# Kernel optimization log

Hardware: AMD Instinct MI355X
Metric: run time of the kernel (lower is better)

The kernel has to match this reference:

```python
import jax, jax.numpy as jnp
import numpy as np

N = 1_000_000   # total points
C = 20          # semantic classes
B = 4           # scenes in batch
L = 200         # instance label vocabulary
INST = 64       # number of proposals/instances
M = 300_000     # masked points (len(object_idxs))
T = 320_000     # total proposal rows
IGNORE = -100
PREPARE_EPOCHS = 128


def setup_inputs() -> dict:
    key = jax.random.key(0)
    ks = jax.random.split(key, 12)
    semantic_scores = jax.random.normal(ks[0], (N, C), jnp.float32)
    semantic_labels = jax.random.randint(ks[1], (N,), 0, C)
    lab = jax.random.randint(ks[2], (N,), 0, L)
    ign = jax.random.uniform(ks[3], (N,)) < 0.05
    instance_labels = jnp.where(ign, IGNORE, lab)
    pt_offsets = jax.random.normal(ks[4], (N, 3), jnp.float32)
    instance_info = jax.random.normal(ks[5], (N, 9), jnp.float32)
    coords = jax.random.normal(ks[6], (N, 3), jnp.float32)
    mask_logits = jax.random.normal(ks[7], (INST, M), jnp.float32)
    object_idxs = jax.random.randint(ks[8], (M,), 0, N)
    col1 = jax.random.randint(ks[9], (T,), 0, N)
    proposals_idx_shift = jnp.stack([jnp.zeros_like(col1), col1], axis=1)
    mids = jnp.sort(jax.random.randint(ks[10], (INST - 1,), 0, T))
    proposals_offset_shift = jnp.concatenate(
        [jnp.zeros((1,), jnp.int32), mids.astype(jnp.int32), jnp.full((1,), T, jnp.int32)])
    inst_batch_ids = jax.random.randint(ks[11], (INST,), 0, B)
    batch_offsets = jnp.array([0, N // 4, N // 2, 3 * N // 4, N], dtype=jnp.int32)
    batch_ids = jnp.clip(jnp.searchsorted(batch_offsets, object_idxs, side='right') - 1, 0, B - 1)
    inst_pred_seg_label = jax.random.randint(jax.random.fold_in(key, 99), (INST,), 0, C)
    return dict(semantic_scores=semantic_scores, pt_offsets=pt_offsets,
                instance_info=instance_info, coords=coords, mask_logits=mask_logits,
                semantic_labels=semantic_labels, instance_labels=instance_labels,
                object_idxs=object_idxs, proposals_idx_shift=proposals_idx_shift,
                proposals_offset_shift=proposals_offset_shift, inst_batch_ids=inst_batch_ids,
                batch_ids=batch_ids, batch_offsets=batch_offsets,
                inst_pred_seg_label=inst_pred_seg_label, epoch=200)


def reference(semantic_scores, pt_offsets, instance_info, coords, mask_logits,
              semantic_labels, instance_labels, object_idxs, proposals_idx_shift,
              proposals_offset_shift, inst_batch_ids, batch_ids, batch_offsets,
              inst_pred_seg_label, epoch):
    f32 = jnp.float32
    n_pts = semantic_scores.shape[0]
    n_inst, m_pts = mask_logits.shape
    n_batch = batch_offsets.shape[0] - 1
    LW = L + 1  # label buckets, bucket 0 == ignore(-100)

    # --- semantic cross entropy (ignore_index) ---
    logp = jax.nn.log_softmax(semantic_scores, axis=-1)
    sem_valid = semantic_labels != IGNORE
    safe_lab = jnp.where(sem_valid, semantic_labels, 0)
    nll = -jnp.take_along_axis(logp, safe_lab[:, None], axis=1)[:, 0]
    semantic_loss = jnp.sum(nll * sem_valid) / jnp.maximum(jnp.sum(sem_valid), 1)

    # --- offset losses ---
    gt_offsets = instance_info[:, 0:3] - coords
    pt_dist = jnp.sum(jnp.abs(pt_offsets - gt_offsets), axis=-1)
    valid = (instance_labels != IGNORE).astype(f32)
    vsum = jnp.sum(valid) + 1e-6
    offset_norm_loss = jnp.sum(pt_dist * valid) / vsum
    gt_u = gt_offsets / (jnp.linalg.norm(gt_offsets, axis=1, keepdims=True) + 1e-8)
    pt_u = pt_offsets / (jnp.linalg.norm(pt_offsets, axis=1, keepdims=True) + 1e-8)
    offset_dir_loss = jnp.sum(-jnp.sum(gt_u * pt_u, axis=-1) * valid) / vsum

    loss = semantic_loss + offset_norm_loss + offset_dir_loss

    if epoch > PREPARE_EPOCHS:
        # map instance labels to ids: ignore -> 0, label l -> l+1 (order-preserving, so
        # argmax-first tie-break == torch.mode smallest-value tie-break)
        labels_id = jnp.where(instance_labels == IGNORE, 0, instance_labels + 1)
        # segment id per proposal row from CSR offsets
        seg = jnp.clip(jnp.searchsorted(proposals_offset_shift, jnp.arange(T), side='right') - 1,
                       0, n_inst - 1)
        prop_lab = labels_id[proposals_idx_shift[:, 1]]
        hist = jax.ops.segment_sum(jnp.ones((T,), f32), seg * LW + prop_lab,
                                   num_segments=n_inst * LW).reshape(n_inst, LW)
        mode_id = jnp.argmax(hist, axis=1)                       # [INST] per-instance mode vote

        masked_lab = labels_id[object_idxs]                      # [M]
        sem_masked = semantic_labels[object_idxs]                # [M]
        skip = (mode_id == 0) | (inst_pred_seg_label <= 3)       # [INST]

        batch_match = inst_batch_ids[:, None] == batch_ids[None, :]           # [INST,M]
        sem_match = inst_pred_seg_label[:, None] == sem_masked[None, :]       # [INST,M]
        weights = batch_match.astype(f32) * jnp.where(skip[:, None], 1.0,
                                                      sem_match.astype(f32))  # [INST,M]

        # per-batch label histograms (full points and masked points)
        point_batch = jnp.clip(jnp.searchsorted(batch_offsets, jnp.arange(n_pts),
                                                side='right') - 1, 0, n_batch - 1)
        hist_full = jax.ops.segment_sum(jnp.ones((n_pts,), f32), point_batch * LW + labels_id,
                                        num_segments=n_batch * LW).reshape(n_batch, LW)
        hist_mask = jax.ops.segment_sum(jnp.ones((m_pts,), f32), batch_ids * LW + masked_lab,
                                        num_segments=n_batch * LW).reshape(n_batch, LW)
        num = hist_mask[inst_batch_ids, mode_id]
        den = hist_full[inst_batch_ids, mode_id]
        cover = jnp.where(den > 0, num / den, 0.0)
        pos = (~skip) & (cover > 0.3)
        inst_gt_mask = (pos[:, None] & (masked_lab[None, :] == mode_id[:, None])).astype(f32)

        pred = jax.nn.sigmoid(mask_logits)
        wb = (weights > 0).astype(f32)
        inter = jnp.sum(wb * pred * inst_gt_mask, axis=1)
        union = jnp.sum(wb * pred * pred, axis=1) + jnp.sum(wb * inst_gt_mask * inst_gt_mask, axis=1) + 1e-5
        dice_n = 1.0 - 2.0 * inter / union
        dice_valid = (~skip) & (jnp.sum(wb, axis=1) > 0)
        dice_loss = jnp.sum(jnp.where(dice_valid, dice_n, 0.0)) / (jnp.sum(dice_valid.astype(f32)) + 1e-6)

        # BCE(sigmoid(x), t) in stable form: softplus(x) - t*x
        bce = jax.nn.softplus(mask_logits) - inst_gt_mask * mask_logits
        score_loss = jnp.sum(bce * weights) / (jnp.sum(weights) + 1e-6)

        loss = loss + score_loss + dice_loss
    return loss
```

## Files before the change

### kernel.cpp

```cpp
#include <hip/hip_runtime.h>
#include <math.h>

namespace {

constexpr int N_PTS  = 1000000;
constexpr int C_CLS  = 20;
constexpr int N_B    = 4;
constexpr int L_LAB  = 200;
constexpr int LW     = L_LAB + 1;
constexpr int N_INST = 64;
constexpr int M_PTS  = 300000;
constexpr int T_PROP = 320000;
constexpr int IGN    = -100;
constexpr int PREP   = 128;

constexpr size_t OFF_G      = 0;
constexpr size_t OFF_INTER  = 64;
constexpr size_t OFF_UP     = 576;
constexpr size_t OFF_UG     = 1088;
constexpr size_t OFF_WBS    = 1600;
constexpr size_t OFF_SN     = 2112;
constexpr size_t OFF_HFULL  = 2624;
constexpr size_t OFF_HMASK  = 5840;
constexpr size_t OFF_IHIST  = 9056;
constexpr size_t OFF_FLAGS  = 60512;
constexpr size_t ZERO_BYTES = 60768;
constexpr size_t OFF_META   = 60800;
constexpr size_t WS_REQUIRED = OFF_META + (size_t)M_PTS * 2;

__device__ __forceinline__ float waveSumF(float v) {
  #pragma unroll
  for (int off = 32; off > 0; off >>= 1) v += __shfl_down(v, off, 64);
  return v;
}
__device__ __forceinline__ int waveMaxI(int v) {
  #pragma unroll
  for (int off = 32; off > 0; off >>= 1) v = max(v, __shfl_down(v, off, 64));
  return v;
}

constexpr int PB_PT   = 1024;
constexpr int PB_HF   = 256;
constexpr int PB_PROP = 256;
constexpr int PB_HM   = 256;
constexpr int A_BLOCKS = PB_PT + PB_HF + PB_PROP + PB_HM;

__global__ __launch_bounds__(256) void k_A(const float* __restrict__ scores,
                                           const float* __restrict__ pt_off,
                                           const float* __restrict__ info,
                                           const float* __restrict__ coords,
                                           const int* __restrict__ sem_lab,
                                           const int* __restrict__ inst_lab,
                                           const int* __restrict__ obj_idx,
                                           const int* __restrict__ batch_ids,
                                           const int* __restrict__ prop_idx,
                                           const int* __restrict__ prop_off,
                                           const int* __restrict__ batch_off,
                                           double* __restrict__ g,
                                           int* __restrict__ hist_full,
                                           int* __restrict__ hist_mask,
                                           int* __restrict__ inst_hist,
                                           unsigned short* __restrict__ meta,
                                           int write_meta) {
  __shared__ float4 shbuf4[4 * 320];
  int*   sh  = reinterpret_cast<int*>(shbuf4);
  float* shf = reinterpret_cast<float*>(shbuf4);
  const int bx = blockIdx.x;

  if (bx < PB_PT) {
    const int lane = threadIdx.x & 63, wv = threadIdx.x >> 6;
    float4* shw4 = shbuf4 + wv * 320;
    float*  shwf = reinterpret_cast<float*>(shw4);
    float s_nll = 0.f, s_cnt = 0.f, s_dist = 0.f, s_dir = 0.f, s_val = 0.f;

    constexpr int NT      = N_PTS / 64;
    constexpr int TSTRIDE = PB_PT * 4;
    const int base = bx * 4 + wv;
    const int nit = (NT - bx * 4 + TSTRIDE - 1) / TSTRIDE;

    for (int it = 0; it < nit; ++it) {
      const int tile = base + it * TSTRIDE;
      const bool act = tile < NT;
      int sl = 0, il = IGN;

      if (act) {
        const int p = tile * 64 + lane;
        sl = sem_lab[p];
        il = inst_lab[p];
        const float4* s4 = reinterpret_cast<const float4*>(scores) + (size_t)tile * 320;
        #pragma unroll
        for (int r = 0; r < 5; ++r) shw4[r * 64 + lane] = s4[r * 64 + lane];
      }
      __syncthreads();

      if (act) {
        float mx = -3.4e38f;
        #pragma unroll
        for (int r = 0; r < 5; ++r) {
          const float4 a = shw4[lane * 5 + r];
          mx = fmaxf(mx, fmaxf(fmaxf(a.x, a.y), fmaxf(a.z, a.w)));
        }
        float se = 0.f;
        #pragma unroll
        for (int r = 0; r < 5; ++r) {
          const float4 a = shw4[lane * 5 + r];
          se += __expf(a.x - mx) + __expf(a.y - mx) + __expf(a.z - mx) + __expf(a.w - mx);
        }
        const float xs = shwf[lane * 20 + ((sl == IGN) ? 0 : sl)];
        if (sl != IGN) { s_nll += (mx + __logf(se)) - xs; s_cnt += 1.f; }
      }
      __syncthreads();

      if (act) {
        const float4* c4 = reinterpret_cast<const float4*>(coords) + (size_t)tile * 48;
        const float4* o4 = reinterpret_cast<const float4*>(pt_off) + (size_t)tile * 48;
        const float4* i4 = reinterpret_cast<const float4*>(info)   + (size_t)tile * 144;
        if (lane < 48) { shw4[lane] = c4[lane]; shw4[48 + lane] = o4[lane]; }
        shw4[96 + lane]  = i4[lane];
        shw4[160 + lane] = i4[64 + lane];
        if (lane < 16) shw4[224 + lane] = i4[128 + lane];
      }
      __syncthreads();

      if (act && il != IGN) {
        const float cx = shwf[3 * lane + 0], cy = shwf[3 * lane + 1], cz = shwf[3 * lane + 2];
        const float ox = shwf[192 + 3 * lane + 0], oy = shwf[192 + 3 * lane + 1], oz = shwf[192 + 3 * lane + 2];
        const float gx = shwf[384 + 9 * lane + 0] - cx;
        const float gy = shwf[384 + 9 * lane + 1] - cy;
        const float gz = shwf[384 + 9 * lane + 2] - cz;
        s_val  += 1.f;
        s_dist += fabsf(ox - gx) + fabsf(oy - gy) + fabsf(oz - gz);
        const float gn = sqrtf(gx * gx + gy * gy + gz * gz) + 1e-8f;
        const float pn = sqrtf(ox * ox + oy * oy + oz * oz) + 1e-8f;
        s_dir += -((gx * ox + gy * oy + gz * oz) / (gn * pn));
      }
      __syncthreads();
    }

    float vals[5] = { s_nll, s_cnt, s_dist, s_dir, s_val };
    #pragma unroll
    for (int k = 0; k < 5; ++k) {
      const float t = waveSumF(vals[k]);
      if (lane == 0) shf[k * 4 + wv] = t;
    }
    __syncthreads();
    if (threadIdx.x < 5) {
      const float s = shf[threadIdx.x * 4 + 0] + shf[threadIdx.x * 4 + 1] +
                      shf[threadIdx.x * 4 + 2] + shf[threadIdx.x * 4 + 3];
      atomicAdd(&g[threadIdx.x], (double)s);
    }
  } else if (bx < PB_PT + PB_HF) {
    for (int t = threadIdx.x; t < N_B * LW; t += blockDim.x) sh[t] = 0;
    __syncthreads();
    const int b1 = batch_off[1], b2 = batch_off[2], b3 = batch_off[3];
    const int blk = bx - PB_PT;
    const int4* il4p = reinterpret_cast<const int4*>(inst_lab);
    const int nq = N_PTS / 4;
    for (int q = blk * blockDim.x + threadIdx.x; q < nq; q += PB_HF * blockDim.x) {
      const int4 v = il4p[q];
      const int p = q * 4;
      const int ils[4] = { v.x, v.y, v.z, v.w };
      #pragma unroll
      for (int k = 0; k < 4; ++k) {
        const int lab = (ils[k] == IGN) ? 0 : (ils[k] + 1);
        const int pp = p + k;
        int pb = 0;
        if (pp >= b1) pb = 1;
        if (pp >= b2) pb = 2;
        if (pp >= b3) pb = 3;
        atomicAdd(&sh[pb * LW + lab], 1);
      }
    }
    __syncthreads();
    for (int t = threadIdx.x; t < N_B * LW; t += blockDim.x)
      if (sh[t]) atomicAdd(&hist_full[t], sh[t]);
  } else if (bx < PB_PT + PB_HF + PB_PROP) {
    if (threadIdx.x <= N_INST) sh[threadIdx.x] = prop_off[threadIdx.x];
    __syncthreads();
    const int blk = bx - PB_PT - PB_HF;
    const int4* pi4 = reinterpret_cast<const int4*>(prop_idx);
    const int nq = T_PROP / 2;
    for (int q = blk * blockDim.x + threadIdx.x; q < nq; q += PB_PROP * blockDim.x) {
      const int4 v = pi4[q];
      const int t0 = 2 * q, t1 = 2 * q + 1;
      const int il0 = inst_lab[v.y];
      const int il1 = inst_lab[v.w];
      int lo0 = 0, hi0 = N_INST + 1, lo1 = 0, hi1 = N_INST + 1;
      #pragma unroll
      for (int s = 0; s < 7; ++s) {
        const int m0 = (lo0 + hi0) >> 1;
        if (m0 <= N_INST && sh[m0] <= t0) lo0 = m0 + 1; else hi0 = m0;
        const int m1 = (lo1 + hi1) >> 1;
        if (m1 <= N_INST && sh[m1] <= t1) lo1 = m1 + 1; else hi1 = m1;
      }
      const int seg0 = min(lo0 - 1, N_INST - 1);
      const int seg1 = min(lo1 - 1, N_INST - 1);
      const int lab0 = (il0 == IGN) ? 0 : (il0 + 1);
      const int lab1 = (il1 == IGN) ? 0 : (il1 + 1);
      atomicAdd(&inst_hist[seg0 * LW + lab0], 1);
      atomicAdd(&inst_hist[seg1 * LW + lab1], 1);
    }
  } else {
    for (int t = threadIdx.x; t < N_B * LW; t += blockDim.x) sh[t] = 0;
    __syncthreads();
    const int blk = bx - PB_PT - PB_HF - PB_PROP;
    const int4* oi4 = reinterpret_cast<const int4*>(obj_idx);
    const int4* bi4 = reinterpret_cast<const int4*>(batch_ids);
    ushort4* m4 = reinterpret_cast<ushort4*>(meta);
    const int nq = M_PTS / 4;
    for (int q = blk * blockDim.x + threadIdx.x; q < nq; q += PB_HM * blockDim.x) {
      const int4 o = oi4[q];
      const int4 b = bi4[q];
      const int il0 = inst_lab[o.x], il1 = inst_lab[o.y],
                il2 = inst_lab[o.z], il3 = inst_lab[o.w];
      const int sm0 = sem_lab[o.x], sm1 = sem_lab[o.y],
                sm2 = sem_lab[o.z], sm3 = sem_lab[o.w];
      const int ml0 = (il0 == IGN) ? 0 : (il0 + 1);
      const int ml1 = (il1 == IGN) ? 0 : (il1 + 1);
      const int ml2 = (il2 == IGN) ? 0 : (il2 + 1);
      const int ml3 = (il3 == IGN) ? 0 : (il3 + 1);
      atomicAdd(&sh[b.x * LW + ml0], 1);
      atomicAdd(&sh[b.y * LW + ml1], 1);
      atomicAdd(&sh[b.z * LW + ml2], 1);
      atomicAdd(&sh[b.w * LW + ml3], 1);
      if (write_meta) {
        ushort4 mm;
        mm.x = (unsigned short)(ml0 | (sm0 << 8) | (b.x << 13));
        mm.y = (unsigned short)(ml1 | (sm1 << 8) | (b.y << 13));
        mm.z = (unsigned short)(ml2 | (sm2 << 8) | (b.z << 13));
        mm.w = (unsigned short)(ml3 | (sm3 << 8) | (b.w << 13));
        m4[q] = mm;
      }
    }
    __syncthreads();
    for (int t = threadIdx.x; t < N_B * LW; t += blockDim.x)
      if (sh[t]) atomicAdd(&hist_mask[t], sh[t]);
  }
}

__global__ __launch_bounds__(256) void k_argmax(const int* __restrict__ inst_hist,
                                                const int* __restrict__ hist_full,
                                                const int* __restrict__ hist_mask,
                                                const int* __restrict__ inst_batch_ids,
                                                const int* __restrict__ inst_seg,
                                                int* __restrict__ flags) {
  __shared__ int red[4];
  const int i = blockIdx.x;
  const int t = threadIdx.x;
  int key = 0;
  if (t < LW) {
    const int cnt = inst_hist[i * LW + t];
    key = (cnt << 8) | (255 - t);
  }
  key = waveMaxI(key);
  const int lane = t & 63, wv = t >> 6;
  if (lane == 0) red[wv] = key;
  __syncthreads();
  if (t == 0) {
    int k = max(max(red[0], red[1]), max(red[2], red[3]));
    const int m = 255 - (k & 0xFF);
    const int b = inst_batch_ids[i];
    const int seg = inst_seg[i];
    const bool skip = (m == 0) || (seg <= 3);
    const float num = (float)hist_mask[b * LW + m];
    const float den = (float)hist_full[b * LW + m];
    const float cover = (den > 0.f) ? (num / den) : 0.f;
    const bool pos = (!skip) && (cover > 0.3f);
    flags[i] = m | (skip ? 0x100 : 0) | (pos ? 0x200 : 0) | (b << 10) | (seg << 12);
  }
}

template <bool USE_META>
__global__ __launch_bounds__(256) void k_mask(const float* __restrict__ logits,
                                              const unsigned short* __restrict__ meta,
                                              const int* __restrict__ obj_idx,
                                              const int* __restrict__ inst_lab,
                                              const int* __restrict__ sem_lab,
                                              const int* __restrict__ batch_ids,
                                              const int* __restrict__ flags,
                                              double* __restrict__ i_inter,
                                              double* __restrict__ i_up,
                                              double* __restrict__ i_ug,
                                              double* __restrict__ i_wbs,
                                              double* __restrict__ i_sn) {
  const int i  = blockIdx.y;
  const int fl = flags[i];
  const int  mode_i = fl & 0xFF;
  const bool skip   = (fl >> 8) & 1;
  const bool pos    = (fl >> 9) & 1;
  const int  bi     = (fl >> 10) & 3;
  const int  seg    = (fl >> 12) & 31;

  float inter = 0.f, up = 0.f, ug = 0.f, wbs = 0.f, sn = 0.f;

  if (USE_META) {
    const float4* row4 = reinterpret_cast<const float4*>(logits + (size_t)i * M_PTS);
    const ushort4* m4  = reinterpret_cast<const ushort4*>(meta);
    const int nq = M_PTS / 4;
    for (int q = blockIdx.x * blockDim.x + threadIdx.x; q < nq; q += gridDim.x * blockDim.x) {
      const float4  x4 = row4[q];
      const ushort4 d4 = m4[q];
      const float xs[4] = { x4.x, x4.y, x4.z, x4.w };
      const int   ds[4] = { d4.x, d4.y, d4.z, d4.w };
      #pragma unroll
      for (int k = 0; k < 4; ++k) {
        const int md = ds[k];
        const int ml = md & 0xFF;
        const int sm = (md >> 8) & 31;
        const int b  = (md >> 13) & 3;
        const bool w  = (b == bi) && (skip || (sm == seg));
        const bool gt = pos && (ml == mode_i);
        const float x  = xs[k];
        const float e  = __expf(-fabsf(x));
        const float r  = __builtin_amdgcn_rcpf(1.f + e);
        const float pr = (x >= 0.f) ? r : e * r;
        const float sp = fmaxf(x, 0.f) + __logf(1.f + e);
        const float wf = w ? 1.f : 0.f;
        const float gf = gt ? 1.f : 0.f;
        up    += wf * pr * pr;
        wbs   += wf;
        sn    += wf * (sp - gf * x);
        inter += wf * gf * pr;
        ug    += wf * gf;
      }
    }
  } else {
    const float* row = logits + (size_t)i * M_PTS;
    for (int j = blockIdx.x * blockDim.x + threadIdx.x; j < M_PTS; j += gridDim.x * blockDim.x) {
      const int o  = obj_idx[j];
      const int il = inst_lab[o];
      const int ml = (il == IGN) ? 0 : (il + 1);
      const int sm = sem_lab[o];
      const int b  = batch_ids[j];
      const bool w  = (b == bi) && (skip || (sm == seg));
      const bool gt = pos && (ml == mode_i);
      const float x  = row[j];
      const float e  = __expf(-fabsf(x));
      const float r  = __builtin_amdgcn_rcpf(1.f + e);
      const float pr = (x >= 0.f) ? r : e * r;
      const float sp = fmaxf(x, 0.f) + __logf(1.f + e);
      const float wf = w ? 1.f : 0.f;
      const float gf = gt ? 1.f : 0.f;
      up    += wf * pr * pr;
      wbs   += wf;
      sn    += wf * (sp - gf * x);
      inter += wf * gf * pr;
      ug    += wf * gf;
    }
  }

  __shared__ float red[5][4];
  float vals[5] = { inter, up, ug, wbs, sn };
  const int lane = threadIdx.x & 63, wv = threadIdx.x >> 6;
  #pragma unroll
  for (int k = 0; k < 5; ++k) {
    const float t = waveSumF(vals[k]);
    if (lane == 0) red[k][wv] = t;
  }
  __syncthreads();
  if (threadIdx.x < 5) {
    const float s = red[threadIdx.x][0] + red[threadIdx.x][1] + red[threadIdx.x][2] + red[threadIdx.x][3];
    double* dst = (threadIdx.x == 0) ? (i_inter + i)
                : (threadIdx.x == 1) ? (i_up + i)
                : (threadIdx.x == 2) ? (i_ug + i)
                : (threadIdx.x == 3) ? (i_wbs + i)
                                     : (i_sn + i);
    atomicAdd(dst, (double)s);
  }
}

__global__ __launch_bounds__(64) void k_final(const double* __restrict__ g,
                                              const double* __restrict__ i_inter,
                                              const double* __restrict__ i_up,
                                              const double* __restrict__ i_ug,
                                              const double* __restrict__ i_wbs,
                                              const double* __restrict__ i_sn,
                                              const int* __restrict__ flags,
                                              const int* __restrict__ epoch,
                                              float* __restrict__ out) {
  const int i = threadIdx.x;
  const bool act = epoch[0] > PREP;
  double sn = 0.0, wsum = 0.0, dice = 0.0, dcnt = 0.0;
  if (act) {
    wsum = i_wbs[i];
    sn   = i_sn[i];
    const bool skip = (flags[i] >> 8) & 1;
    if (!skip && wsum > 0.0) {
      const double un = i_up[i] + i_ug[i] + 1e-5;
      dice = 1.0 - 2.0 * i_inter[i] / un;
      dcnt = 1.0;
    }
    #pragma unroll
    for (int off = 32; off > 0; off >>= 1) {
      wsum += __shfl_down(wsum, off, 64);
      sn   += __shfl_down(sn,   off, 64);
      dice += __shfl_down(dice, off, 64);
      dcnt += __shfl_down(dcnt, off, 64);
    }
  }
  if (i == 0) {
    double loss = g[0] / fmax(g[1], 1.0);
    const double vsum = g[4] + 1e-6;
    loss += g[2] / vsum + g[3] / vsum;
    if (act) loss += sn / (wsum + 1e-6) + dice / (dcnt + 1e-6);
    out[0] = (float)loss;
  }
}

}

extern "C" void kernel_launch(void* const* d_in, const int* in_sizes, int n_in,
                              void* d_out, int out_size, void* d_ws, size_t ws_size,
                              hipStream_t stream) {
  const float* semantic_scores  = (const float*)d_in[0];
  const float* pt_offsets       = (const float*)d_in[1];
  const float* instance_info    = (const float*)d_in[2];
  const float* coords           = (const float*)d_in[3];
  const float* mask_logits      = (const float*)d_in[4];
  const int*   semantic_labels  = (const int*)d_in[5];
  const int*   instance_labels  = (const int*)d_in[6];
  const int*   object_idxs      = (const int*)d_in[7];
  const int*   proposals_idx    = (const int*)d_in[8];
  const int*   proposals_off    = (const int*)d_in[9];
  const int*   inst_batch_ids   = (const int*)d_in[10];
  const int*   batch_ids        = (const int*)d_in[11];
  const int*   batch_offsets    = (const int*)d_in[12];
  const int*   inst_seg         = (const int*)d_in[13];
  const int*   epoch            = (const int*)d_in[14];
  float* out = (float*)d_out;

  char* w = (char*)d_ws;
  double* g        = (double*)(w + OFF_G);
  double* i_inter  = (double*)(w + OFF_INTER);
  double* i_up     = (double*)(w + OFF_UP);
  double* i_ug     = (double*)(w + OFF_UG);
  double* i_wbs    = (double*)(w + OFF_WBS);
  double* i_sn     = (double*)(w + OFF_SN);
  int* hist_full   = (int*)(w + OFF_HFULL);
  int* hist_mask   = (int*)(w + OFF_HMASK);
  int* inst_hist   = (int*)(w + OFF_IHIST);
  int* flags       = (int*)(w + OFF_FLAGS);
  unsigned short* meta = (unsigned short*)(w + OFF_META);

  const bool use_meta = (ws_size >= WS_REQUIRED);

  (void)hipMemsetAsync(d_ws, 0, ZERO_BYTES, stream);

  k_A<<<A_BLOCKS, 256, 0, stream>>>(semantic_scores, pt_offsets, instance_info, coords,
                                    semantic_labels, instance_labels, object_idxs,
                                    batch_ids, proposals_idx, proposals_off, batch_offsets,
                                    g, hist_full, hist_mask, inst_hist, meta,
                                    use_meta ? 1 : 0);

  k_argmax<<<N_INST, 256, 0, stream>>>(inst_hist, hist_full, hist_mask,
                                       inst_batch_ids, inst_seg, flags);

  dim3 mgrid(40, N_INST);
  if (use_meta) {
    k_mask<true><<<mgrid, 256, 0, stream>>>(mask_logits, meta, object_idxs, instance_labels,
                                            semantic_labels, batch_ids, flags,
                                            i_inter, i_up, i_ug, i_wbs, i_sn);
  } else {
    k_mask<false><<<mgrid, 256, 0, stream>>>(mask_logits, meta, object_idxs, instance_labels,
                                             semantic_labels, batch_ids, flags,
                                             i_inter, i_up, i_ug, i_wbs, i_sn);
  }
  k_final<<<1, 64, 0, stream>>>(g, i_inter, i_up, i_ug, i_wbs, i_sn, flags, epoch, out);
}
```

Measured before the change: 273.7 us.

## Drop per-tile block barriers in point loop and replace double atomics with partials

The point-loss blocks now give each wave its own shared-memory region holding scores, coords, offsets and info together. This removes the four block-wide __syncthreads per tile, since each wave reads only its own data. Each point block writes its five partial sums to a workspace array instead of doing double-precision atomicAdds, and the final kernel grows to 256 threads to reduce those partials. Shared memory per block rises, which may lower occupancy. Correctness relies on wave-level execution ordering for the intra-wave shared-memory handoff.

```diff
diff --git a/kernel.cpp b/kernel.cpp
--- a/kernel.cpp
+++ b/kernel.cpp
@@ -25,7 +25,10 @@
 constexpr size_t OFF_IHIST  = 9056;
 constexpr size_t OFF_FLAGS  = 60512;
 constexpr size_t ZERO_BYTES = 60768;
-constexpr size_t OFF_META   = 60800;
+constexpr size_t OFF_PART   = 60800;
+constexpr size_t PART_BYTES = 5 * 1024 * 4;
+constexpr size_t WS_PART_REQ = OFF_PART + PART_BYTES;
+constexpr size_t OFF_META   = WS_PART_REQ;
 constexpr size_t WS_REQUIRED = OFF_META + (size_t)M_PTS * 2;
 
 __device__ __forceinline__ float waveSumF(float v) {
@@ -44,6 +47,8 @@
 constexpr int PB_PROP = 256;
 constexpr int PB_HM   = 256;
 constexpr int A_BLOCKS = PB_PT + PB_HF + PB_PROP + PB_HM;
+
+constexpr int WREG = 560;
 
 __global__ __launch_bounds__(256) void k_A(const float* __restrict__ scores,
                                            const float* __restrict__ pt_off,
@@ -57,19 +62,21 @@
                                            const int* __restrict__ prop_off,
                                            const int* __restrict__ batch_off,
                                            double* __restrict__ g,
+                                           float* __restrict__ part,
+                                           int use_part,
                                            int* __restrict__ hist_full,
                                            int* __restrict__ hist_mask,
                                            int* __restrict__ inst_hist,
                                            unsigned short* __restrict__ meta,
                                            int write_meta) {
-  __shared__ float4 shbuf4[4 * 320];
+  __shared__ float4 shbuf4[4 * WREG];
   int*   sh  = reinterpret_cast<int*>(shbuf4);
   float* shf = reinterpret_cast<float*>(shbuf4);
   const int bx = blockIdx.x;
 
   if (bx < PB_PT) {
     const int lane = threadIdx.x & 63, wv = threadIdx.x >> 6;
-    float4* shw4 = shbuf4 + wv * 320;
+    float4* shw4 = shbuf4 + wv * WREG;
     float*  shwf = reinterpret_cast<float*>(shw4);
     float s_nll = 0.f, s_cnt = 0.f, s_dist = 0.f, s_dir = 0.f, s_val = 0.f;
 
@@ -80,20 +87,22 @@
 
     for (int it = 0; it < nit; ++it) {
       const int tile = base + it * TSTRIDE;
-      const bool act = tile < NT;
-      int sl = 0, il = IGN;
-
-      if (act) {
+      if (tile < NT) {
         const int p = tile * 64 + lane;
-        sl = sem_lab[p];
-        il = inst_lab[p];
+        const int sl = sem_lab[p];
+        const int il = inst_lab[p];
+
         const float4* s4 = reinterpret_cast<const float4*>(scores) + (size_t)tile * 320;
         #pragma unroll
         for (int r = 0; r < 5; ++r) shw4[r * 64 + lane] = s4[r * 64 + lane];
-      }
-      __syncthreads();
-
-      if (act) {
+        const float4* c4 = reinterpret_cast<const float4*>(coords) + (size_t)tile * 48;
+        const float4* o4 = reinterpret_cast<const float4*>(pt_off) + (size_t)tile * 48;
+        const float4* i4 = reinterpret_cast<const float4*>(info)   + (size_t)tile * 144;
+        if (lane < 48) { shw4[320 + lane] = c4[lane]; shw4[368 + lane] = o4[lane]; }
+        shw4[416 + lane] = i4[lane];
+        shw4[480 + lane] = i4[64 + lane];
+        if (lane < 16) shw4[544 + lane] = i4[128 + lane];
+
         float mx = -3.4e38f;
         #pragma unroll
         for (int r = 0; r < 5; ++r) {
@@ -108,35 +117,27 @@
         }
         const float xs = shwf[lane * 20 + ((sl == IGN) ? 0 : sl)];
         if (sl != IGN) { s_nll += (mx + __logf(se)) - xs; s_cnt += 1.f; }
-      }
-      __syncthreads();
-
-      if (act) {
-        const float4* c4 = reinterpret_cast<const float4*>(coords) + (size_t)tile * 48;
-        const float4* o4 = reinterpret_cast<const float4*>(pt_off) + (size_t)tile * 48;
-        const float4* i4 = reinterpret_cast<const float4*>(info)   + (size_t)tile * 144;
-        if (lane < 48) { shw4[lane] = c4[lane]; shw4[48 + lane] = o4[lane]; }
-        shw4[96 + lane]  = i4[lane];
-        shw4[160 + lane] = i4[64 + lane];
-        if (lane < 16) shw4[224 + lane] = i4[128 + lane];
-      }
-      __syncthreads();
-
-      if (act && il != IGN) {
-        const float cx = shwf[3 * lane + 0], cy = shwf[3 * lane + 1], cz = shwf[3 * lane + 2];
-        const float ox = shwf[192 + 3 * lane + 0], oy = shwf[192 + 3 * lane + 1], oz = shwf[192 + 3 * lane + 2];
-        const float gx = shwf[384 + 9 * lane + 0] - cx;
-        const float gy = shwf[384 + 9 * lane + 1] - cy;
-        const float gz = shwf[384 + 9 * lane + 2] - cz;
-        s_val  += 1.f;
-        s_dist += fabsf(ox - gx) + fabsf(oy - gy) + fabsf(oz - gz);
-        const float gn = sqrtf(gx * gx + gy * gy + gz * gz) + 1e-8f;
-        const float pn = sqrtf(ox * ox + oy * oy + oz * oz) + 1e-8f;
-        s_dir += -((gx * ox + gy * oy + gz * oz) / (gn * pn));
-      }
-      __syncthreads();
-    }
-
+
+        if (il != IGN) {
+          const float cx = shwf[1280 + 3 * lane + 0];
+          const float cy = shwf[1280 + 3 * lane + 1];
+          const float cz = shwf[1280 + 3 * lane + 2];
+          const float ox = shwf[1472 + 3 * lane + 0];
+          const float oy = shwf[1472 + 3 * lane + 1];
+          const float oz = shwf[1472 + 3 * lane + 2];
+          const float gx = shwf[1664 + 9 * lane + 0] - cx;
+          const float gy = shwf[1664 + 9 * lane + 1] - cy;
+          const float gz = shwf[1664 + 9 * lane + 2] - cz;
+          s_val  += 1.f;
+          s_dist += fabsf(ox - gx) + fabsf(oy - gy) + fabsf(oz - gz);
+          const float gn = sqrtf(gx * gx + gy * gy + gz * gz) + 1e-8f;
+          const float pn = sqrtf(ox * ox + oy * oy + oz * oz) + 1e-8f;
+          s_dir += -((gx * ox + gy * oy + gz * oz) / (gn * pn));
+        }
+      }
+    }
+
+    __syncthreads();
     float vals[5] = { s_nll, s_cnt, s_dist, s_dir, s_val };
     #pragma unroll
     for (int k = 0; k < 5; ++k) {
@@ -147,7 +148,8 @@
     if (threadIdx.x < 5) {
       const float s = shf[threadIdx.x * 4 + 0] + shf[threadIdx.x * 4 + 1] +
                       shf[threadIdx.x * 4 + 2] + shf[threadIdx.x * 4 + 3];
-      atomicAdd(&g[threadIdx.x], (double)s);
+      if (use_part) part[threadIdx.x * PB_PT + bx] = s;
+      else          atomicAdd(&g[threadIdx.x], (double)s);
     }
   } else if (bx < PB_PT + PB_HF) {
     for (int t = threadIdx.x; t < N_B * LW; t += blockDim.x) sh[t] = 0;
@@ -369,40 +371,66 @@
   }
 }
 
-__global__ __launch_bounds__(64) void k_final(const double* __restrict__ g,
-                                              const double* __restrict__ i_inter,
-                                              const double* __restrict__ i_up,
-                                              const double* __restrict__ i_ug,
-                                              const double* __restrict__ i_wbs,
-                                              const double* __restrict__ i_sn,
-                                              const int* __restrict__ flags,
-                                              const int* __restrict__ epoch,
-                                              float* __restrict__ out) {
-  const int i = threadIdx.x;
+__global__ __launch_bounds__(256) void k_final(const double* __restrict__ g,
+                                               const float* __restrict__ part,
+                                               int use_part,
+                                               const double* __restrict__ i_inter,
+                                               const double* __restrict__ i_up,
+                                               const double* __restrict__ i_ug,
+                                               const double* __restrict__ i_wbs,
+                                               const double* __restrict__ i_sn,
+                                               const int* __restrict__ flags,
+                                               const int* __restrict__ epoch,
+                                               float* __restrict__ out) {
+  __shared__ double sred[5][4];
+  __shared__ double sG[5];
+  __shared__ double sI[4];
+  const int t = threadIdx.x, lane = t & 63, wv = t >> 6;
+
+  if (use_part) {
+    #pragma unroll
+    for (int c = 0; c < 5; ++c) {
+      double v = 0.0;
+      #pragma unroll
+      for (int j = 0; j < 4; ++j) v += (double)part[c * 1024 + t + j * 256];
+      #pragma unroll
+      for (int off = 32; off > 0; off >>= 1) v += __shfl_down(v, off, 64);
+      if (lane == 0) sred[c][wv] = v;
+    }
+    __syncthreads();
+    if (t < 5) sG[t] = sred[t][0] + sred[t][1] + sred[t][2] + sred[t][3];
+  } else {
+    if (t < 5) sG[t] = g[t];
+  }
+
   const bool act = epoch[0] > PREP;
-  double sn = 0.0, wsum = 0.0, dice = 0.0, dcnt = 0.0;
-  if (act) {
-    wsum = i_wbs[i];
-    sn   = i_sn[i];
-    const bool skip = (flags[i] >> 8) & 1;
-    if (!skip && wsum > 0.0) {
-      const double un = i_up[i] + i_ug[i] + 1e-5;
-      dice = 1.0 - 2.0 * i_inter[i] / un;
-      dcnt = 1.0;
-    }
-    #pragma unroll
-    for (int off = 32; off > 0; off >>= 1) {
-      wsum += __shfl_down(wsum, off, 64);
-      sn   += __shfl_down(sn,   off, 64);
-      dice += __shfl_down(dice, off, 64);
-      dcnt += __shfl_down(dcnt, off, 64);
-    }
-  }
-  if (i == 0) {
-    double loss = g[0] / fmax(g[1], 1.0);
-    const double vsum = g[4] + 1e-6;
-    loss += g[2] / vsum + g[3] / vsum;
-    if (act) loss += sn / (wsum + 1e-6) + dice / (dcnt + 1e-6);
+  if (t < 64) {
+    double sn = 0.0, wsum = 0.0, dice = 0.0, dcnt = 0.0;
+    if (act) {
+      wsum = i_wbs[t];
+      sn   = i_sn[t];
+      const bool skip = (flags[t] >> 8) & 1;
+      if (!skip && wsum > 0.0) {
+        const double un = i_up[t] + i_ug[t] + 1e-5;
+        dice = 1.0 - 2.0 * i_inter[t] / un;
+        dcnt = 1.0;
+      }
+      #pragma unroll
+      for (int off = 32; off > 0; off >>= 1) {
+        wsum += __shfl_down(wsum, off, 64);
+        sn   += __shfl_down(sn,   off, 64);
+        dice += __shfl_down(dice, off, 64);
+        dcnt += __shfl_down(dcnt, off, 64);
+      }
+    }
+    if (t == 0) { sI[0] = sn; sI[1] = wsum; sI[2] = dice; sI[3] = dcnt; }
+  }
+  __syncthreads();
+  if (t == 0) {
+    double loss = sG[0] / fmax(sG[1], 1.0);
+    const double vsum = sG[4] + 1e-6;
+    loss += sG[2] / vsum + sG[3] / vsum;
+    if (act) loss += sI[0] / (sI[1] + 1e-6) + sI[2] / (sI[3] + 1e-6);
     out[0] = (float)loss;
   }
 }
@@ -440,8 +468,10 @@
   int* hist_mask   = (int*)(w + OFF_HMASK);
   int* inst_hist   = (int*)(w + OFF_IHIST);
   int* flags       = (int*)(w + OFF_FLAGS);
+  float* part      = (float*)(w + OFF_PART);
   unsigned short* meta = (unsigned short*)(w + OFF_META);
 
+  const bool use_part = (ws_size >= WS_PART_REQ);
   const bool use_meta = (ws_size >= WS_REQUIRED);
 
   (void)hipMemsetAsync(d_ws, 0, ZERO_BYTES, stream);
@@ -449,7 +479,8 @@
   k_A<<<A_BLOCKS, 256, 0, stream>>>(semantic_scores, pt_offsets, instance_info, coords,
                                     semantic_labels, instance_labels, object_idxs,
                                     batch_ids, proposals_idx, proposals_off, batch_offsets,
-                                    g, hist_full, hist_mask, inst_hist, meta,
+                                    g, part, use_part ? 1 : 0,
+                                    hist_full, hist_mask, inst_hist, meta,
                                     use_meta ? 1 : 0);
 
   k_argmax<<<N_INST, 256, 0, stream>>>(inst_hist, hist_full, hist_mask,
@@ -465,5 +496,6 @@
                                              semantic_labels, batch_ids, flags,
                                              i_inter, i_up, i_ug, i_wbs, i_sn);
   }
-  k_final<<<1, 64, 0, stream>>>(g, i_inter, i_up, i_ug, i_wbs, i_sn, flags, epoch, out);
-}
+  k_final<<<1, 256, 0, stream>>>(g, part, use_part ? 1 : 0,
+                                 i_inter, i_up, i_ug, i_wbs, i_sn, flags, epoch, out);
+}
```

Result: slower. 293.4 us (+7.2%).
